# Optimization experiments

Measured on AMD Instinct MI355X. Metric: run time of the kernel, lower is better.

Reference implementation:

```python
import jax, jax.numpy as jnp
import numpy as np

N, S, F, D = 4096, 128, 128, 256  # batch, memory slots, feat_dim, dim_h_o
EPS = 1e-8  # torch CosineSimilarity eps


def _xavier(key, shape):
    fan_out, fan_in = shape
    std = float(np.sqrt(2.0 / (fan_in + fan_out)))
    return jax.random.normal(key, shape, dtype=jnp.float32) * std


def setup_inputs() -> dict:
    key = jax.random.key(0)
    ks = jax.random.split(key, 10)
    return {
        "h_o_prev": jax.random.normal(ks[0], (N, D), dtype=jnp.float32),
        "C": jax.random.normal(ks[1], (N, S, F), dtype=jnp.float32),
        "Wk": _xavier(ks[2], (F, D)), "bk": jnp.zeros((F,), jnp.float32),
        "Wb": _xavier(ks[3], (1, D)), "bb": jnp.zeros((1,), jnp.float32),
        "We": _xavier(ks[4], (F, D)), "be": jnp.zeros((F,), jnp.float32),
        "Wv": _xavier(ks[5], (F, D)), "bv": jnp.zeros((F,), jnp.float32),
        "Wih": _xavier(ks[6], (3 * D, F)), "Whh": _xavier(ks[7], (3 * D, D)),
        "bih": jnp.zeros((3 * D,), jnp.float32), "bhh": jnp.zeros((3 * D,), jnp.float32),
    }


def reference(h_o_prev, C, Wk, bk, Wb, bb, We, be, Wv, bv, Wih, Whh, bih, bhh):
    # --- Attention (content addressing) ---
    k = h_o_prev @ Wk.T + bk                              # [N, F]
    beta_pre = h_o_prev @ Wb.T + bb                       # [N, 1]
    # clamp-split softplus trick in source == softplus(x) + 1
    beta = jax.nn.softplus(beta_pre) + 1.0                # [N, 1]
    C_norm = jnp.maximum(jnp.linalg.norm(C, axis=2), EPS)           # [N, S]
    k_norm = jnp.maximum(jnp.linalg.norm(k, axis=1, keepdims=True), EPS)  # [N, 1]
    s = jnp.einsum("nsf,nf->ns", C, k) / (C_norm * k_norm)          # cosine sim [N, S]
    w = jax.nn.softmax(s * beta, axis=1)                  # [N, S]
    # --- Read memory ---
    r = jnp.einsum("ns,nsf->nf", w, C)                    # [N, F]
    # --- GRU cell update (torch GRUCell semantics) ---
    gi = r @ Wih.T + bih                                  # [N, 3D]
    gh = h_o_prev @ Whh.T + bhh                           # [N, 3D]
    i_r, i_z, i_n = jnp.split(gi, 3, axis=1)
    h_r, h_z, h_n = jnp.split(gh, 3, axis=1)
    rg = jax.nn.sigmoid(i_r + h_r)
    z = jax.nn.sigmoid(i_z + h_z)
    n = jnp.tanh(i_n + rg * h_n)
    h_o = (1.0 - z) * n + z * h_o_prev                    # [N, D]
    # --- Write memory (erase + add, outer products) ---
    e = jax.nn.sigmoid(h_o @ We.T + be)                   # [N, F]
    v = h_o @ Wv.T + bv                                   # [N, F]
    w2 = w[:, :, None]                                    # [N, S, 1]
    C_new = C * (1.0 - w2 * e[:, None, :]) + w2 * v[:, None, :]
    return h_o, C_new, k, r
```

## Files before the change

kernel.cpp:

```cpp
#include <hip/hip_runtime.h>
#include <hip/hip_bf16.h>
#include <cstddef>
#include <cstdint>

constexpr int Nn = 4096;
constexpr int Ss = 128;
constexpr int Ff = 128;
constexpr int Dd = 256;
constexpr float EPSV = 1e-8f;

constexpr size_t HO_OFF = 0;
constexpr size_t C_OFF  = (size_t)Nn * Dd;
constexpr size_t K_OFF  = C_OFF + (size_t)Nn * Ss * Ff;
constexpr size_t R_OFF  = K_OFF + (size_t)Nn * Ff;

typedef __attribute__((ext_vector_type(4))) float f4v;
typedef __attribute__((ext_vector_type(8))) short bh8;
typedef __attribute__((ext_vector_type(4))) short bh4;

constexpr int WK_O  = 0;
constexpr int WHH_O = 32768;
constexpr int WIH_O = 229376;
constexpr int WEV_O = 327680;
constexpr int W_TOT = 393216;

__device__ __forceinline__ float sigmf(float x) { return 1.0f / (1.0f + __expf(-x)); }

__device__ __forceinline__ short f2bf(float x) {
    __hip_bfloat16 h = __float2bfloat16(x);
    return *reinterpret_cast<short*>(&h);
}

__device__ __forceinline__ int swzH(int row, int kb) { return row * 512 + (kb ^ ((row & 7) << 4)); }
__device__ __forceinline__ int swzR(int row, int kb) { return row * 256 + (kb ^ ((row & 7) << 4)); }

__device__ __forceinline__ f4v mfma16(bh8 a, bh8 b, f4v c) {
    return __builtin_amdgcn_mfma_f32_16x16x32_bf16(a, b, c, 0, 0, 0);
}

__global__ __launch_bounds__(256) void prep_weights(
    const float* __restrict__ Wk, const float* __restrict__ Whh,
    const float* __restrict__ Wih, const float* __restrict__ We,
    const float* __restrict__ Wv, short* __restrict__ out)
{
    int id = blockIdx.x * 256 + threadIdx.x;
    float v;
    if      (id < WHH_O) v = Wk[id - WK_O];
    else if (id < WIH_O) v = Whh[id - WHH_O];
    else if (id < WEV_O) v = Wih[id - WIH_O];
    else if (id < WEV_O + 32768) v = We[id - WEV_O];
    else v = Wv[id - WEV_O - 32768];
    out[id] = f2bf(v);
}

__global__ __launch_bounds__(512, 4) void mega_kernel(
    const float* __restrict__ C, const float* __restrict__ h_prev,
    const short* __restrict__ WB,
    const float* __restrict__ Wb, const float* __restrict__ bb,
    const float* __restrict__ bk, const float* __restrict__ bhh,
    const float* __restrict__ bih, const float* __restrict__ be,
    const float* __restrict__ bv,
    float* __restrict__ ho, float* __restrict__ Cnew,
    float* __restrict__ kout, float* __restrict__ rout)
{
    __shared__ float sH[8][256];
    __shared__ __align__(16) short sHb[16 * 256];
    __shared__ __align__(16) short sRb[16 * 128];
    __shared__ float sK[8][128];
    __shared__ float sSc[8][128];
    __shared__ float sEV[8][256];

    const int t  = threadIdx.x;
    const int l  = t & 63;
    const int wv = t >> 6;
    const int nb = blockIdx.x * 8;
    char* hb = (char*)sHb;
    char* rb = (char*)sRb;

    const short* WkB  = WB + WK_O;
    const short* WhhB = WB + WHH_O;
    const short* WihB = WB + WIH_O;
    const short* WevB = WB + WEV_O;

    {
        const int f = t * 4, row = f >> 8, col = f & 255;
        float4 hv = *(const float4*)(h_prev + (size_t)(nb + row) * Dd + col);
        *(float4*)&sH[row][col] = hv;
        bh4 hb4 = { f2bf(hv.x), f2bf(hv.y), f2bf(hv.z), f2bf(hv.w) };
        *(bh4*)(hb + swzH(row, col * 2)) = hb4;
        *(int64_t*)(hb + 4096 + t * 8) = 0;
        *(int*)(rb + 2048 + t * 4) = 0;
    }
    __syncthreads();

    {
        const int fr = l & 15, kq = l >> 4, rbase = kq * 4;
        const int colg = wv * 16 + fr;
        f4v acc = {0.f, 0.f, 0.f, 0.f};
#pragma unroll
        for (int kc = 0; kc < 8; ++kc) {
            bh8 a = *(const bh8*)(hb + swzH(fr, kc * 64 + kq * 16));
            bh8 b = *(const bh8*)(WkB + (size_t)colg * 256 + kc * 32 + kq * 8);
            acc = mfma16(a, b, acc);
        }
        if (rbase < 8) {
            const float bs = bk[colg];
#pragma unroll
            for (int rg = 0; rg < 4; ++rg) {
                float x = acc[rg] + bs;
                sK[rbase + rg][colg] = x;
                kout[(size_t)(nb + rbase + rg) * Ff + colg] = x;
            }
        }
    }
    __syncthreads();

    float invL_r = 0.0f;
    {
        const float* Cn = C + (size_t)(nb + wv) * (Ss * Ff);

        float kv0 = sK[wv][l], kv1 = sK[wv][64 + l];
        float ks = kv0 * kv0 + kv1 * kv1;
#pragma unroll
        for (int o = 32; o > 0; o >>= 1) ks += __shfl_xor(ks, o);
        const float knorm = fmaxf(sqrtf(ks), EPSV);

        float4 hv = *(const float4*)&sH[wv][l * 4];
        float4 wb4 = *(const float4*)(Wb + l * 4);
        float bp = hv.x * wb4.x + hv.y * wb4.y + hv.z * wb4.z + hv.w * wb4.w;
#pragma unroll
        for (int o = 32; o > 0; o >>= 1) bp += __shfl_xor(bp, o);
        bp += bb[0];
        const float beta = ((bp > 20.0f) ? bp : log1pf(__expf(bp))) + 1.0f;
        const float bOkn = beta / knorm;

        const int qrow = l >> 2;
        const int subf = l & 3;
        const int half = l >> 5, fl = l & 31, f4 = fl * 4;
        float lsum = 0.0f;
        f4v racc = {0.f, 0.f, 0.f, 0.f};

#pragma unroll 1
        for (int tile = 0; tile < 8; ++tile) {
            const int s0 = tile * 16;
            const float* rowp = Cn + (size_t)(s0 + qrow) * Ff + subf * 32;
            float d = 0.f, q = 0.f;
#pragma unroll
            for (int fc = 0; fc < 8; ++fc) {
                const f4v c4 = *(const f4v*)(rowp + fc * 4);
                const f4v k4 = *(const f4v*)&sK[wv][subf * 32 + fc * 4];
                d += c4.x * k4.x + c4.y * k4.y + c4.z * k4.z + c4.w * k4.w;
                q += c4.x * c4.x + c4.y * c4.y + c4.z * c4.z + c4.w * c4.w;
            }
            d += __shfl_xor(d, 1); d += __shfl_xor(d, 2);
            q += __shfl_xor(q, 1); q += __shfl_xor(q, 2);
            const float x = d / fmaxf(sqrtf(q), EPSV) * bOkn;
            const float p = __expf(x - beta);
            if (subf == 0) sSc[wv][s0 + qrow] = p;
            lsum += p;
#pragma unroll
            for (int j = 0; j < 8; ++j) {
                const int s = s0 + j * 2 + half;
                const float pp = sSc[wv][s];
                const f4v c4 = *(const f4v*)(Cn + (size_t)s * Ff + f4);
                racc += pp * c4;
            }
        }
#pragma unroll
        for (int o = 32; o > 0; o >>= 1) lsum += __shfl_xor(lsum, o);
        const float iL = 4.0f / lsum;
        invL_r = iL;

        f4v r2;
        r2.x = __shfl_xor(racc.x, 32); r2.y = __shfl_xor(racc.y, 32);
        r2.z = __shfl_xor(racc.z, 32); r2.w = __shfl_xor(racc.w, 32);
        f4v r4 = (racc + r2) * iL;
        if (half == 0) {
            *(f4v*)(rout + (size_t)(nb + wv) * Ff + f4) = r4;
            bh4 rb4 = { f2bf(r4.x), f2bf(r4.y), f2bf(r4.z), f2bf(r4.w) };
            *(bh4*)(rb + swzR(wv, f4 * 2)) = rb4;
        }
    }
    __syncthreads();

    {
        const int fr = l & 15, kq = l >> 4, rbase = kq * 4;
        float hoReg[2][4];
#pragma unroll
        for (int dp = 0; dp < 2; ++dp) {
            f4v aG[3], aI[3];
#pragma unroll
            for (int gi = 0; gi < 3; ++gi) {
                const int colg = (gi * 2 + dp) * 128 + wv * 16 + fr;
                f4v g = {0.f, 0.f, 0.f, 0.f}, ii = {0.f, 0.f, 0.f, 0.f};
#pragma unroll
                for (int kc = 0; kc < 8; ++kc) {
                    bh8 a = *(const bh8*)(hb + swzH(fr, kc * 64 + kq * 16));
                    bh8 b = *(const bh8*)(WhhB + (size_t)colg * 256 + kc * 32 + kq * 8);
                    g = mfma16(a, b, g);
                }
#pragma unroll
                for (int kc = 0; kc < 4; ++kc) {
                    bh8 a = *(const bh8*)(rb + swzR(fr, kc * 64 + kq * 16));
                    bh8 b = *(const bh8*)(WihB + (size_t)colg * 128 + kc * 32 + kq * 8);
                    ii = mfma16(a, b, ii);
                }
                aG[gi] = g; aI[gi] = ii;
            }
            if (rbase < 8) {
                const int d = dp * 128 + wv * 16 + fr;
                const float br  = bhh[d] + bih[d];
                const float bz  = bhh[256 + d] + bih[256 + d];
                const float bhn = bhh[512 + d];
                const float bin = bih[512 + d];
#pragma unroll
                for (int rg = 0; rg < 4; ++rg) {
                    const float rgt = sigmf(aG[0][rg] + aI[0][rg] + br);
                    const float z   = sigmf(aG[1][rg] + aI[1][rg] + bz);
                    const float nn  = tanhf(aI[2][rg] + bin + rgt * (aG[2][rg] + bhn));
                    const float hp  = sH[rbase + rg][d];
                    hoReg[dp][rg] = (1.0f - z) * nn + z * hp;
                }
            }
        }
        __syncthreads();
        if (rbase < 8) {
#pragma unroll
            for (int dp = 0; dp < 2; ++dp) {
                const int d = dp * 128 + wv * 16 + fr;
#pragma unroll
                for (int rg = 0; rg < 4; ++rg) {
                    const int row = rbase + rg;
                    const float o = hoReg[dp][rg];
                    ho[(size_t)(nb + row) * Dd + d] = o;
                    *(short*)(hb + row * 512 + ((d * 2) ^ ((row & 7) << 4))) = f2bf(o);
                }
            }
        }
    }
    __syncthreads();

    {
        const int fr = l & 15, kq = l >> 4, rbase = kq * 4;
#pragma unroll
        for (int i = 0; i < 2; ++i) {
            const int colg = i * 128 + wv * 16 + fr;
            f4v acc = {0.f, 0.f, 0.f, 0.f};
#pragma unroll
            for (int kc = 0; kc < 8; ++kc) {
                bh8 a = *(const bh8*)(hb + swzH(fr, kc * 64 + kq * 16));
                bh8 b = *(const bh8*)(WevB + (size_t)colg * 256 + kc * 32 + kq * 8);
                acc = mfma16(a, b, acc);
            }
            if (rbase < 8) {
                const float bs = (colg < 128) ? be[colg] : bv[colg - 128];
#pragma unroll
                for (int rg = 0; rg < 4; ++rg) {
                    float x = acc[rg] + bs;
                    if (colg < 128) x = sigmf(x);
                    sEV[rbase + rg][colg] = x;
                }
            }
        }
    }
    __syncthreads();

    {
        const int half = l >> 5, fl = l & 31, f4 = fl * 4;
        const float* Cn = C    + (size_t)(nb + wv) * (Ss * Ff);
        float*       Co = Cnew + (size_t)(nb + wv) * (Ss * Ff);
        const f4v e4 = *(const f4v*)&sEV[wv][f4];
        const f4v v4 = *(const f4v*)&sEV[wv][128 + f4];
        const float iL = invL_r;

#pragma unroll 4
        for (int k = 0; k < 64; ++k) {
            const int s = k * 2 + half;
            const f4v c4 = *(const f4v*)(Cn + (size_t)s * Ff + f4);
            const float wsc = sSc[wv][s] * iL;
            f4v o = c4 * (1.0f - wsc * e4) + wsc * v4;
            __builtin_nontemporal_store(o, (f4v*)(Co + (size_t)s * Ff + f4));
        }
    }
}

extern "C" void kernel_launch(void* const* d_in, const int* in_sizes, int n_in,
                              void* d_out, int out_size, void* d_ws, size_t ws_size,
                              hipStream_t stream)
{
    const float* h_prev = (const float*)d_in[0];
    const float* C      = (const float*)d_in[1];
    const float* Wk     = (const float*)d_in[2];
    const float* bk     = (const float*)d_in[3];
    const float* Wb     = (const float*)d_in[4];
    const float* bb     = (const float*)d_in[5];
    const float* We     = (const float*)d_in[6];
    const float* be     = (const float*)d_in[7];
    const float* Wv     = (const float*)d_in[8];
    const float* bv     = (const float*)d_in[9];
    const float* Wih    = (const float*)d_in[10];
    const float* Whh    = (const float*)d_in[11];
    const float* bih    = (const float*)d_in[12];
    const float* bhh    = (const float*)d_in[13];

    float* out  = (float*)d_out;
    float* ho   = out + HO_OFF;
    float* Cnew = out + C_OFF;
    float* kbuf = out + K_OFF;
    float* rbuf = out + R_OFF;

    short* wsB = (short*)d_ws;

    prep_weights<<<W_TOT / 256, 256, 0, stream>>>(Wk, Whh, Wih, We, Wv, wsB);

    mega_kernel<<<Nn / 8, 512, 0, stream>>>(
        C, h_prev, wsB, Wb, bb, bk, bhh, bih, be, bv,
        ho, Cnew, kbuf, rbuf);
}
```

Measured before the change: 192.9 us.

## Halve rows per block to 4 with 256-thread blocks, doubling column tiles per wave

Each block now handles 4 batch rows with 4 waves instead of 8 rows with 8 waves, and the grid doubles to 1024 blocks. Each wave now covers two or four column tiles in the MFMA stages, and only the kq==0 lanes hold valid rows because of the 16-row MFMA padding. This gives more, smaller blocks for better CU load balance and less LDS per block. In exchange, 12 of the 16 MFMA rows are now padding instead of 8, so the matrix work per useful row rises and each weight load is amortised over fewer rows.

```diff
diff --git a/kernel.cpp b/kernel.cpp
--- a/kernel.cpp
+++ b/kernel.cpp
@@ -53,7 +53,7 @@
     out[id] = f2bf(v);
 }
 
-__global__ __launch_bounds__(512, 4) void mega_kernel(
+__global__ __launch_bounds__(256, 2) void mega_kernel(
     const float* __restrict__ C, const float* __restrict__ h_prev,
     const short* __restrict__ WB,
     const float* __restrict__ Wb, const float* __restrict__ bb,
@@ -63,17 +63,17 @@
     float* __restrict__ ho, float* __restrict__ Cnew,
     float* __restrict__ kout, float* __restrict__ rout)
 {
-    __shared__ float sH[8][256];
+    __shared__ float sH[4][256];
     __shared__ __align__(16) short sHb[16 * 256];
     __shared__ __align__(16) short sRb[16 * 128];
-    __shared__ float sK[8][128];
-    __shared__ float sSc[8][128];
-    __shared__ float sEV[8][256];
+    __shared__ float sK[4][128];
+    __shared__ float sSc[4][128];
+    __shared__ float sEV[4][256];
 
     const int t  = threadIdx.x;
     const int l  = t & 63;
     const int wv = t >> 6;
-    const int nb = blockIdx.x * 8;
+    const int nb = blockIdx.x * 4;
     char* hb = (char*)sHb;
     char* rb = (char*)sRb;
 
@@ -88,28 +88,34 @@
         *(float4*)&sH[row][col] = hv;
         bh4 hb4 = { f2bf(hv.x), f2bf(hv.y), f2bf(hv.z), f2bf(hv.w) };
         *(bh4*)(hb + swzH(row, col * 2)) = hb4;
-        *(int64_t*)(hb + 4096 + t * 8) = 0;
-        *(int*)(rb + 2048 + t * 4) = 0;
-    }
-    __syncthreads();
-
-    {
-        const int fr = l & 15, kq = l >> 4, rbase = kq * 4;
-        const int colg = wv * 16 + fr;
-        f4v acc = {0.f, 0.f, 0.f, 0.f};
-#pragma unroll
-        for (int kc = 0; kc < 8; ++kc) {
-            bh8 a = *(const bh8*)(hb + swzH(fr, kc * 64 + kq * 16));
-            bh8 b = *(const bh8*)(WkB + (size_t)colg * 256 + kc * 32 + kq * 8);
-            acc = mfma16(a, b, acc);
-        }
-        if (rbase < 8) {
-            const float bs = bk[colg];
-#pragma unroll
-            for (int rg = 0; rg < 4; ++rg) {
-                float x = acc[rg] + bs;
-                sK[rbase + rg][colg] = x;
-                kout[(size_t)(nb + rbase + rg) * Ff + colg] = x;
+        *(int4*)(hb + 2048 + t * 16) = int4{0, 0, 0, 0};
+        *(int64_t*)(hb + 6144 + t * 8) = 0;
+        *(int64_t*)(rb + 1024 + t * 8) = 0;
+        *(int*)(rb + 3072 + t * 4) = 0;
+    }
+    __syncthreads();
+
+    const int fr = l & 15, kq = l >> 4;
+
+    {
+#pragma unroll
+        for (int i = 0; i < 2; ++i) {
+            const int colg = i * 64 + wv * 16 + fr;
+            f4v acc = {0.f, 0.f, 0.f, 0.f};
+#pragma unroll
+            for (int kc = 0; kc < 8; ++kc) {
+                bh8 a = *(const bh8*)(hb + swzH(fr, kc * 64 + kq * 16));
+                bh8 b = *(const bh8*)(WkB + (size_t)colg * 256 + kc * 32 + kq * 8);
+                acc = mfma16(a, b, acc);
+            }
+            if (kq == 0) {
+                const float bs = bk[colg];
+#pragma unroll
+                for (int rg = 0; rg < 4; ++rg) {
+                    float x = acc[rg] + bs;
+                    sK[rg][colg] = x;
+                    kout[(size_t)(nb + rg) * Ff + colg] = x;
+                }
             }
         }
     }
@@ -184,67 +190,69 @@
     __syncthreads();
 
     {
-        const int fr = l & 15, kq = l >> 4, rbase = kq * 4;
-        float hoReg[2][4];
+        float hoReg[2][2][4];
 #pragma unroll
         for (int dp = 0; dp < 2; ++dp) {
-            f4v aG[3], aI[3];
-#pragma unroll
-            for (int gi = 0; gi < 3; ++gi) {
-                const int colg = (gi * 2 + dp) * 128 + wv * 16 + fr;
-                f4v g = {0.f, 0.f, 0.f, 0.f}, ii = {0.f, 0.f, 0.f, 0.f};
-#pragma unroll
-                for (int kc = 0; kc < 8; ++kc) {
-                    bh8 a = *(const bh8*)(hb + swzH(fr, kc * 64 + kq * 16));
-                    bh8 b = *(const bh8*)(WhhB + (size_t)colg * 256 + kc * 32 + kq * 8);
-                    g = mfma16(a, b, g);
-                }
-#pragma unroll
-                for (int kc = 0; kc < 4; ++kc) {
-                    bh8 a = *(const bh8*)(rb + swzR(fr, kc * 64 + kq * 16));
-                    bh8 b = *(const bh8*)(WihB + (size_t)colg * 128 + kc * 32 + kq * 8);
-                    ii = mfma16(a, b, ii);
-                }
-                aG[gi] = g; aI[gi] = ii;
-            }
-            if (rbase < 8) {
-                const int d = dp * 128 + wv * 16 + fr;
-                const float br  = bhh[d] + bih[d];
-                const float bz  = bhh[256 + d] + bih[256 + d];
-                const float bhn = bhh[512 + d];
-                const float bin = bih[512 + d];
-#pragma unroll
-                for (int rg = 0; rg < 4; ++rg) {
-                    const float rgt = sigmf(aG[0][rg] + aI[0][rg] + br);
-                    const float z   = sigmf(aG[1][rg] + aI[1][rg] + bz);
-                    const float nn  = tanhf(aI[2][rg] + bin + rgt * (aG[2][rg] + bhn));
-                    const float hp  = sH[rbase + rg][d];
-                    hoReg[dp][rg] = (1.0f - z) * nn + z * hp;
+#pragma unroll
+            for (int cs = 0; cs < 2; ++cs) {
+                f4v aG[3], aI[3];
+#pragma unroll
+                for (int g3 = 0; g3 < 3; ++g3) {
+                    const int colg = (g3 * 2 + dp) * 128 + cs * 64 + wv * 16 + fr;
+                    f4v g = {0.f, 0.f, 0.f, 0.f}, ii = {0.f, 0.f, 0.f, 0.f};
+#pragma unroll
+                    for (int kc = 0; kc < 8; ++kc) {
+                        bh8 a = *(const bh8*)(hb + swzH(fr, kc * 64 + kq * 16));
+                        bh8 b = *(const bh8*)(WhhB + (size_t)colg * 256 + kc * 32 + kq * 8);
+                        g = mfma16(a, b, g);
+                    }
+#pragma unroll
+                    for (int kc = 0; kc < 4; ++kc) {
+                        bh8 a = *(const bh8*)(rb + swzR(fr, kc * 64 + kq * 16));
+                        bh8 b = *(const bh8*)(WihB + (size_t)colg * 128 + kc * 32 + kq * 8);
+                        ii = mfma16(a, b, ii);
+                    }
+                    aG[g3] = g; aI[g3] = ii;
+                }
+                if (kq == 0) {
+                    const int d = dp * 128 + cs * 64 + wv * 16 + fr;
+                    const float br  = bhh[d] + bih[d];
+                    const float bz  = bhh[256 + d] + bih[256 + d];
+                    const float bhn = bhh[512 + d];
+                    const float bin = bih[512 + d];
+#pragma unroll
+                    for (int rg = 0; rg < 4; ++rg) {
+                        const float rgt = sigmf(aG[0][rg] + aI[0][rg] + br);
+                        const float z   = sigmf(aG[1][rg] + aI[1][rg] + bz);
+                        const float nn  = tanhf(aI[2][rg] + bin + rgt * (aG[2][rg] + bhn));
+                        const float hp  = sH[rg][d];
+                        hoReg[dp][cs][rg] = (1.0f - z) * nn + z * hp;
+                    }
                 }
             }
         }
         __syncthreads();
-        if (rbase < 8) {
-#pragma unroll
-            for (int dp = 0; dp < 2; ++dp) {
-                const int d = dp * 128 + wv * 16 + fr;
-#pragma unroll
-                for (int rg = 0; rg < 4; ++rg) {
-                    const int row = rbase + rg;
-                    const float o = hoReg[dp][rg];
-                    ho[(size_t)(nb + row) * Dd + d] = o;
-                    *(short*)(hb + row * 512 + ((d * 2) ^ ((row & 7) << 4))) = f2bf(o);
-                }
-            }
-        }
-    }
-    __syncthreads();
-
-    {
-        const int fr = l & 15, kq = l >> 4, rbase = kq * 4;
-#pragma unroll
-        for (int i = 0; i < 2; ++i) {
-            const int colg = i * 128 + wv * 16 + fr;
+        if (kq == 0) {
+#pragma unroll
+            for (int dp = 0; dp < 2; ++dp)
+#pragma unroll
+                for (int cs = 0; cs < 2; ++cs) {
+                    const int d = dp * 128 + cs * 64 + wv * 16 + fr;
+#pragma unroll
+                    for (int rg = 0; rg < 4; ++rg) {
+                        const float o = hoReg[dp][cs][rg];
+                        ho[(size_t)(nb + rg) * Dd + d] = o;
+                        *(short*)(hb + rg * 512 + ((d * 2) ^ ((rg & 7) << 4))) = f2bf(o);
+                    }
+                }
+        }
+    }
+    __syncthreads();
+
+    {
+#pragma unroll
+        for (int i = 0; i < 4; ++i) {
+            const int colg = i * 64 + wv * 16 + fr;
             f4v acc = {0.f, 0.f, 0.f, 0.f};
 #pragma unroll
             for (int kc = 0; kc < 8; ++kc) {
@@ -252,13 +260,13 @@
                 bh8 b = *(const bh8*)(WevB + (size_t)colg * 256 + kc * 32 + kq * 8);
                 acc = mfma16(a, b, acc);
             }
-            if (rbase < 8) {
+            if (kq == 0) {
                 const float bs = (colg < 128) ? be[colg] : bv[colg - 128];
 #pragma unroll
                 for (int rg = 0; rg < 4; ++rg) {
                     float x = acc[rg] + bs;
                     if (colg < 128) x = sigmf(x);
-                    sEV[rbase + rg][colg] = x;
+                    sEV[rg][colg] = x;
                 }
             }
         }
@@ -313,7 +321,7 @@
 
     prep_weights<<<W_TOT / 256, 256, 0, stream>>>(Wk, Whh, Wih, We, Wv, wsB);
 
-    mega_kernel<<<Nn / 8, 512, 0, stream>>>(
+    mega_kernel<<<Nn / 4, 256, 0, stream>>>(
         C, h_prev, wsB, Wb, bb, bk, bhh, bih, be, bv,
         ho, Cnew, kbuf, rbuf);
 }
```

New measurement: 230.5 us. 19.5% more time.
